# Performance work log

Hardware: AMD Instinct MI355X
Metric: run time of the kernel (lower is better)

## Reference

```python
import jax, jax.numpy as jnp
import numpy as np

B, N, CZ, CH, CA, H, TN = 1, 256, 128, 128, 32, 4, 4


def setup_inputs() -> dict:
    key = jax.random.key(0)
    ks = iter(jax.random.split(key, 64))

    def rn(shape, s=0.02):
        return jax.random.normal(next(ks), shape, dtype=jnp.float32) * s

    d = {"z": jax.random.normal(next(ks), (B, N, N, CZ), dtype=jnp.float32)}
    # Triangle multiplication params, stacked [2, ...]: idx 0 = outgoing, 1 = incoming
    d["tm_ln_in_w"] = jnp.ones((2, CZ)); d["tm_ln_in_b"] = jnp.zeros((2, CZ))
    for nm, shp in [("ap", (2, CZ, CH)), ("ag", (2, CZ, CH)), ("bp", (2, CZ, CH)),
                    ("bg", (2, CZ, CH)), ("g", (2, CZ, CZ)), ("zo", (2, CH, CZ))]:
        d[f"tm_{nm}_w"] = rn(shp)
        d[f"tm_{nm}_b"] = jnp.zeros((2, shp[-1]))
    d["tm_lnout_w"] = jnp.ones((2, CH)); d["tm_lnout_b"] = jnp.zeros((2, CH))
    # Triangle attention params, stacked [2, ...]: idx 0 = start, 1 = end
    d["ta_ln_w"] = jnp.ones((2, CZ)); d["ta_ln_b"] = jnp.zeros((2, CZ))
    d["ta_q_w"] = rn((2, CZ, H * CA)); d["ta_k_w"] = rn((2, CZ, H * CA)); d["ta_v_w"] = rn((2, CZ, H * CA))
    d["ta_b_w"] = rn((2, CZ, H))
    d["ta_g_w"] = rn((2, CZ, H * CA)); d["ta_g_b"] = jnp.zeros((2, H * CA))
    d["ta_o_w"] = rn((2, H * CA, CZ)); d["ta_o_b"] = jnp.zeros((2, CZ))
    # Pair transition
    d["pt_ln_w"] = jnp.ones((CZ,)); d["pt_ln_b"] = jnp.zeros((CZ,))
    d["pt_1_w"] = rn((CZ, TN * CZ)); d["pt_1_b"] = jnp.zeros((TN * CZ,))
    d["pt_2_w"] = rn((TN * CZ, CZ)); d["pt_2_b"] = jnp.zeros((CZ,))
    return d


def _ln(x, w, b, eps=1e-5):
    m = jnp.mean(x, axis=-1, keepdims=True)
    v = jnp.mean(jnp.square(x - m), axis=-1, keepdims=True)
    return (x - m) * jax.lax.rsqrt(v + eps) * w + b


def _tri_mul(z, lnw, lnb, apw, apb, agw, agb, bpw, bpb, bgw, bgb, gw, gb,
             lnow, lnob, zw, zb, outgoing):
    x = _ln(z, lnw, lnb)
    a = jax.nn.sigmoid(x @ agw + agb) * (x @ apw + apb)  # [B,I,J,CH]
    b = jax.nn.sigmoid(x @ bgw + bgb) * (x @ bpw + bpb)
    eq = 'bikc,bjkc->bijc' if outgoing else 'bkic,bkjc->bijc'
    t = jnp.einsum(eq, a, b)  # O(N^3 * CH)
    t = _ln(t, lnow, lnob) @ zw + zb
    return t * jax.nn.sigmoid(x @ gw + gb)


def _tri_att(z, lnw, lnb, qw, kw, vw, bw, gw, gb, ow, ob):
    Bz, I, J, _ = z.shape
    x = _ln(z, lnw, lnb)
    # triangle bias [B,1,H,I,J] (broadcast over query row)
    bias = jnp.einsum('bijc,ch->bhij', x, bw)[:, None]
    q = (x @ qw).reshape(Bz, I, J, H, CA).transpose(0, 1, 3, 2, 4) / np.float32(np.sqrt(CA))
    k = (x @ kw).reshape(Bz, I, J, H, CA).transpose(0, 1, 3, 2, 4)
    v = (x @ vw).reshape(Bz, I, J, H, CA).transpose(0, 1, 3, 2, 4)
    a = jnp.einsum('bihqc,bihkc->bihqk', q, k) + bias  # [B,I,H,J,J]
    p = jax.nn.softmax(a, axis=-1)
    o = jnp.einsum('bihqk,bihkc->bihqc', p, v).transpose(0, 1, 3, 2, 4).reshape(Bz, I, J, H * CA)
    o = o * jax.nn.sigmoid(x @ gw + gb)
    return o @ ow + ob


def reference(z, tm_ln_in_w, tm_ln_in_b, tm_ap_w, tm_ap_b, tm_ag_w, tm_ag_b,
              tm_bp_w, tm_bp_b, tm_bg_w, tm_bg_b, tm_g_w, tm_g_b,
              tm_lnout_w, tm_lnout_b, tm_zo_w, tm_zo_b,
              ta_ln_w, ta_ln_b, ta_q_w, ta_k_w, ta_v_w, ta_b_w,
              ta_g_w, ta_g_b, ta_o_w, ta_o_b,
              pt_ln_w, pt_ln_b, pt_1_w, pt_1_b, pt_2_w, pt_2_b):
    def tm(zz, i, outgoing):
        return _tri_mul(zz, tm_ln_in_w[i], tm_ln_in_b[i], tm_ap_w[i], tm_ap_b[i],
                        tm_ag_w[i], tm_ag_b[i], tm_bp_w[i], tm_bp_b[i],
                        tm_bg_w[i], tm_bg_b[i], tm_g_w[i], tm_g_b[i],
                        tm_lnout_w[i], tm_lnout_b[i], tm_zo_w[i], tm_zo_b[i], outgoing)

    def ta(zz, i):
        return _tri_att(zz, ta_ln_w[i], ta_ln_b[i], ta_q_w[i], ta_k_w[i], ta_v_w[i],
                        ta_b_w[i], ta_g_w[i], ta_g_b[i], ta_o_w[i], ta_o_b[i])

    z = z + tm(z, 0, True)          # triangle mult outgoing + residual (dropout = eval identity)
    z = z + tm(z, 1, False)         # triangle mult incoming + residual
    z = z + ta(z, 0)                # triangle attention (starting node)
    zt = jnp.swapaxes(z, 1, 2)      # transpose for ending-node attention
    zt = zt + ta(zt, 1)
    z = jnp.swapaxes(zt, 1, 2)
    x = _ln(z, pt_ln_w, pt_ln_b)    # pair transition
    z = z + (jax.nn.relu(x @ pt_1_w + pt_1_b) @ pt_2_w + pt_2_b)
    return z
```

## Files before the change

kernel.cpp:

```cpp
#include <hip/hip_runtime.h>
#include <math.h>

#define N_  256
#define NN  65536
#define CZ  128
#define CH  128
#define H_  4
#define CA  32

typedef __attribute__((ext_vector_type(8))) short bf16x8;
typedef __attribute__((ext_vector_type(4))) float f32x4;

__device__ __forceinline__ float sigmoidf_(float x){ return 1.f/(1.f+__expf(-x)); }

__device__ __forceinline__ short f2b(float f){
  unsigned u = __float_as_uint(f);
  unsigned r = (u + 0x7fffu + ((u>>16)&1u)) >> 16;
  return (short)r;
}
__device__ __forceinline__ float b2f(short s){
  unsigned u = ((unsigned)(unsigned short)s) << 16;
  return __uint_as_float(u);
}
__device__ __forceinline__ unsigned pk_bf16(float lo, float hi){
  unsigned r;
  asm volatile("v_cvt_pk_bf16_f32 %0, %1, %2" : "=v"(r) : "v"(lo), "v"(hi));
  return r;
}

__device__ __forceinline__ void glds16(const void* g, const void* l){
  __builtin_amdgcn_global_load_lds((const __attribute__((address_space(1))) void*)g,
                                   (__attribute__((address_space(3))) void*)l, 16, 0, 0);
}

__device__ __forceinline__ float wave_red_sum(float v){
  #pragma unroll
  for(int o=32;o>0;o>>=1) v += __shfl_xor(v,o,64);
  return v;
}

__device__ __forceinline__ int Gperm(int t, int m){
  return ((t>>1)<<5) + ((m>>2)<<3) + ((t&1)<<2) + (m&3);
}

__global__ void __launch_bounds__(256) prep_weights(
    const float* tm_ag, const float* tm_ap, const float* tm_bg, const float* tm_bp,
    const float* tm_g, const float* tm_zo,
    const float* ta_q, const float* ta_k, const float* ta_v, const float* ta_g, const float* ta_o,
    const float* pt1, const float* pt2, short* Wf){
  int tid = threadIdx.x;
  int g = blockIdx.x*4 + (tid>>6);
  int l = tid & 63;
  int s = blockIdx.y;
  const float* src; int ldn = 128, koff = 0, noff = 0;
  if (s < 12){
    int i = s/6, w = s - i*6;
    switch(w){ case 0: src=tm_ag; break; case 1: src=tm_ap; break; case 2: src=tm_bg; break;
               case 3: src=tm_bp; break; case 4: src=tm_g;  break; default: src=tm_zo; }
    src += i*16384;
  } else if (s < 22){
    int t2 = s-12; int i = t2/5, w = t2 - i*5;
    switch(w){ case 0: src=ta_q; break; case 1: src=ta_k; break; case 2: src=ta_v; break;
               case 3: src=ta_g; break; default: src=ta_o; }
    src += i*16384;
  } else if (s < 26){
    src = pt1; ldn = 512; noff = (s-22)*128;
  } else {
    src = pt2; koff = (s-26)*128;
  }
  int nt = g>>2, ks = g&3;
  int n = noff + nt*16 + (l&15);
  int kb = koff + ks*32 + (l>>4)*8;
  short tmp[8];
  #pragma unroll
  for (int e=0;e<8;e++) tmp[e] = f2b(src[(size_t)(kb+e)*ldn + n]);
  short* dst = Wf + s*16384 + ((nt*4+ks)*64 + l)*8;
  *(short4*)dst     = *(short4*)&tmp[0];
  *(short4*)(dst+4) = *(short4*)&tmp[4];
}

template<bool TRANS>
__global__ void __launch_bounds__(256) ln_x(const float* __restrict__ in,
                                            const float* __restrict__ w,
                                            const float* __restrict__ b,
                                            short* __restrict__ out){
  int wid  = threadIdx.x >> 6;
  int lane = threadIdx.x & 63;
  int row  = blockIdx.x*4 + wid;
  int irow;
  if (TRANS){ int i = row >> 8, j = row & 255; irow = (j<<8) | i; } else irow = row;
  float v0 = in[(size_t)irow*CZ + lane];
  float v1 = in[(size_t)irow*CZ + lane + 64];
  float m  = wave_red_sum(v0+v1) * (1.f/128.f);
  float d0 = v0-m, d1 = v1-m;
  float var = wave_red_sum(d0*d0 + d1*d1) * (1.f/128.f);
  float r = rsqrtf(var + 1e-5f);
  out[(size_t)row*CZ + lane]      = f2b(d0*r*w[lane]    + b[lane]);
  out[(size_t)row*CZ + lane + 64] = f2b(d1*r*w[lane+64] + b[lane+64]);
}

__device__ __forceinline__ void stage128_8(const short* __restrict__ g, short* xs, int r0, int tid){
  #pragma unroll
  for (int m=0;m<4;++m){
    int d = m*512 + tid;
    int row = d>>4, cw = d&15;
    glds16(&g[(size_t)(r0+row)*128 + ((cw ^ (row&15))<<3)], xs + (size_t)(d & ~63)*8);
  }
}

__device__ __forceinline__ bf16x8 ldsA(const short* xs, int row, int ch){
  return *(const bf16x8*)&xs[row*128 + ((ch ^ (row&15))<<3)];
}

__device__ __forceinline__ void gemm_coreP(const short* xs, const short* __restrict__ wf,
                                           int wm, int wn, int l, f32x4 (&acc)[2][4]){
  #pragma unroll
  for (int kh=0; kh<2; ++kh){
    bf16x8 b[2][4];
    #pragma unroll
    for (int ks2=0; ks2<2; ++ks2)
      #pragma unroll
      for (int nt=0; nt<4; ++nt)
        b[ks2][nt] = *(const bf16x8*)&wf[(((wn*4+nt)*4 + kh*2+ks2)*64 + l)*8];
    #pragma unroll
    for (int ks2=0; ks2<2; ++ks2){
      bf16x8 a[2];
      #pragma unroll
      for (int mt=0; mt<2; ++mt)
        a[mt] = ldsA(xs, wm*32 + mt*16 + (l&15), (kh*2+ks2)*4 + (l>>4));
      #pragma unroll
      for (int mt=0; mt<2; ++mt)
        #pragma unroll
        for (int nt=0; nt<4; ++nt)
          acc[mt][nt] = __builtin_amdgcn_mfma_f32_16x16x32_bf16(a[mt], b[ks2][nt], acc[mt][nt], 0,0,0);
    }
  }
}

#define ZERO_ACC(A) { _Pragma("unroll") for(int _a=0;_a<2;_a++) _Pragma("unroll") for(int _b=0;_b<4;_b++) A[_a][_b]=(f32x4){0,0,0,0}; }

#define GEMM_PROLOG8 \
  int tid = threadIdx.x; int r0 = blockIdx.x*128; \
  int wid = tid>>6, l = tid&63; int wm = wid>>1, wn = wid&1; (void)r0;

#define EPI8 \
  int row = wm*32 + mt*16 + ((l>>4)<<2) + reg; \
  int col = wn*64 + nt*16 + (l&15);

#define FOR_EPI for (int mt=0;mt<2;++mt) for (int nt=0;nt<4;++nt) for (int reg=0;reg<4;++reg)

__global__ void __launch_bounds__(512,4) k_quad_gate(const short* __restrict__ X,
                                                     const short* __restrict__ Wagf, const float* __restrict__ bag,
                                                     const short* __restrict__ Wapf, const float* __restrict__ bap,
                                                     const short* __restrict__ Wbgf, const float* __restrict__ bbg,
                                                     const short* __restrict__ Wbpf, const float* __restrict__ bbp,
                                                     short* __restrict__ out1, short* __restrict__ out2){
  __shared__ short xs[128*128];
  GEMM_PROLOG8
  stage128_8(X, xs, r0, tid);
  __syncthreads();
  {
    f32x4 ag[2][4], ap[2][4];
    ZERO_ACC(ag) ZERO_ACC(ap)
    gemm_coreP(xs, Wagf, wm, wn, l, ag);
    gemm_coreP(xs, Wapf, wm, wn, l, ap);
    FOR_EPI{
      EPI8
      float v = (ap[mt][nt][reg] + bap[col]) * sigmoidf_(ag[mt][nt][reg] + bag[col]);
      out1[(size_t)(r0+row)*128 + col] = f2b(v);
    }
  }
  {
    f32x4 bg2[2][4], bp2[2][4];
    ZERO_ACC(bg2) ZERO_ACC(bp2)
    gemm_coreP(xs, Wbgf, wm, wn, l, bg2);
    gemm_coreP(xs, Wbpf, wm, wn, l, bp2);
    FOR_EPI{
      EPI8
      float v = (bp2[mt][nt][reg] + bbp[col]) * sigmoidf_(bg2[mt][nt][reg] + bbg[col]);
      out2[(size_t)(r0+row)*128 + col] = f2b(v);
    }
  }
}

__global__ void __launch_bounds__(512,4) k_qkv(const short* __restrict__ X,
                                               const short* __restrict__ Wqf, float sq,
                                               const short* __restrict__ Wkf,
                                               const short* __restrict__ Wvf,
                                               const float* __restrict__ bw,
                                               short* __restrict__ out_q, short* __restrict__ out_k,
                                               short* __restrict__ Vt, float* __restrict__ BSF){
  __shared__ short xs[128*128];
  GEMM_PROLOG8
  stage128_8(X, xs, r0, tid);
  __syncthreads();
  {
    f32x4 aq[2][4], ak[2][4];
    ZERO_ACC(aq) ZERO_ACC(ak)
    gemm_coreP(xs, Wqf, wm, wn, l, aq);
    gemm_coreP(xs, Wkf, wm, wn, l, ak);
    FOR_EPI{
      EPI8
      out_q[(size_t)(r0+row)*128 + col] = f2b(aq[mt][nt][reg]*sq);
      out_k[(size_t)(r0+row)*128 + col] = f2b(ak[mt][nt][reg]);
    }
  }
  f32x4 av[2][4];
  ZERO_ACC(av)
  gemm_coreP(xs, Wvf, wm, wn, l, av);
  {
    int rl = tid & 127, hh = tid >> 7;
    float bacc = 0.f;
    #pragma unroll
    for (int ch=0; ch<16; ++ch){
      bf16x8 v = ldsA(xs, rl, ch);
      #pragma unroll
      for (int e=0;e<8;++e) bacc += b2f(v[e]) * bw[(ch*8+e)*H_ + hh];
    }
    int r = r0 + rl;
    int qq = r >> 8, j = r & 255;
    int t = ((j>>5)<<1) + ((j>>2)&1);
    int mm = (((j>>3)&3)<<2) + (j&3);
    int idx = (((hh*16 + (qq>>4))*16 + t) << 8) + (((mm>>2)*16 + (qq&15)) << 2) + (mm&3);
    BSF[idx] = bacc;
  }
  __syncthreads();
  #pragma unroll
  for (int mt=0;mt<2;++mt)
    #pragma unroll
    for (int nt=0;nt<4;++nt){
      int rb  = wm*32 + mt*16 + ((l>>4)<<2);
      int col = wn*64 + nt*16 + (l&15);
      short4 s4 = { f2b(av[mt][nt][0]), f2b(av[mt][nt][1]), f2b(av[mt][nt][2]), f2b(av[mt][nt][3]) };
      *(short4*)&xs[col*128 + (((rb>>3) ^ (col&15))<<3) + (rb&7)] = s4;
    }
  __syncthreads();
  int i = r0>>8, j0 = r0&255;
  #pragma unroll
  for (int m=0;m<4;++m){
    int d = m*512 + tid;
    int c = d>>4, ch = d&15;
    int4 val = *(const int4*)&xs[c*128 + ((ch ^ (c&15))<<3)];
    *(int4*)&Vt[(size_t)((i*4 + (c>>5))*32 + (c&31))*256 + j0 + ch*8] = val;
  }
}

__global__ void __launch_bounds__(512,4) k_tri_finish(const short* __restrict__ Tb,
                                                      const short* __restrict__ X,
                                                      const short* __restrict__ Wzf, const float* __restrict__ bz,
                                                      const short* __restrict__ Wgf, const float* __restrict__ bg,
                                                      const float* __restrict__ lnw, const float* __restrict__ lnb,
                                                      const float* __restrict__ zin, float* __restrict__ zout){
  __shared__ short tt[128*128];
  __shared__ short xs[128*128];
  __shared__ float ps[512], pq[512];
  __shared__ float mu[128], iv[128];
  GEMM_PROLOG8
  stage128_8(X, xs, r0, tid);
  #pragma unroll
  for (int m=0;m<4;++m){
    int d = m*512 + tid;
    int c = d>>4, ch = d&15;
    glds16(&Tb[(size_t)c*65536 + r0 + ch*8], tt + (size_t)(d & ~63)*8);
  }
  __syncthreads();
  int rl = tid & 127, cq = tid >> 7;
  float vals[32]; float s = 0.f, q = 0.f;
  #pragma unroll
  for (int cc=0; cc<32; ++cc){
    float v = b2f(tt[(cq*32+cc)*128 + rl]);
    vals[cc] = v; s += v; q += v*v;
  }
  ps[cq*128 + rl] = s; pq[cq*128 + rl] = q;
  __syncthreads();
  if (tid < 128){
    float ss = ps[tid]+ps[128+tid]+ps[256+tid]+ps[384+tid];
    float qq = pq[tid]+pq[128+tid]+pq[256+tid]+pq[384+tid];
    float m = ss * (1.f/128.f);
    float var = qq * (1.f/128.f) - m*m;
    mu[tid] = m; iv[tid] = rsqrtf(var + 1e-5f);
  }
  __syncthreads();
  {
    float m = mu[rl], r = iv[rl];
    #pragma unroll
    for (int chq=0; chq<4; ++chq){
      short tmp[8];
      #pragma unroll
      for (int e=0;e<8;++e){
        int cc = chq*8 + e;
        int c = cq*32 + cc;
        tmp[e] = f2b((vals[cc]-m)*r*lnw[c] + lnb[c]);
      }
      int ch = cq*4 + chq;
      *(int4*)&tt[rl*128 + ((ch ^ (rl&15))<<3)] = *(int4*)tmp;
    }
  }
  __syncthreads();
  f32x4 az[2][4], ag[2][4];
  ZERO_ACC(az) ZERO_ACC(ag)
  gemm_coreP(tt, Wzf, wm, wn, l, az);
  gemm_coreP(xs, Wgf, wm, wn, l, ag);
  FOR_EPI{
    EPI8
    size_t idx = (size_t)(r0+row)*128 + col;
    float v = (az[mt][nt][reg] + bz[col]) * sigmoidf_(ag[mt][nt][reg] + bg[col]);
    zout[idx] = zin[idx] + v;
  }
}

template<bool TRANS>
__global__ void __launch_bounds__(512,4) k_attn_out(const short* __restrict__ O,
                                                    const short* __restrict__ X,
                                                    const short* __restrict__ Wgf, const float* __restrict__ bg,
                                                    const short* __restrict__ Wof, const float* __restrict__ bo,
                                                    float* __restrict__ z){
  __shared__ short xs[128*128];
  __shared__ short os[128*128];
  GEMM_PROLOG8
  stage128_8(X, xs, r0, tid);
  #pragma unroll
  for (int m=0;m<4;++m){
    int d = m*512 + tid;
    int row = d>>4, ch = d&15;
    glds16(&O[(size_t)(r0+row)*128 + ch*8], os + (size_t)(d & ~63)*8);
  }
  __syncthreads();
  f32x4 ag[2][4];
  ZERO_ACC(ag)
  gemm_coreP(xs, Wgf, wm, wn, l, ag);
  __syncthreads();
  FOR_EPI{
    EPI8
    float ov = b2f(os[row*128 + col]);
    float v = ov * sigmoidf_(ag[mt][nt][reg] + bg[col]);
    xs[row*128 + (((col>>3) ^ (row&15))<<3) + (col&7)] = f2b(v);
  }
  __syncthreads();
  f32x4 a2[2][4];
  ZERO_ACC(a2)
  gemm_coreP(xs, Wof, wm, wn, l, a2);
  FOR_EPI{
    EPI8
    int orow = r0+row;
    int zrow = TRANS ? (((orow&255)<<8) | (orow>>8)) : orow;
    z[(size_t)zrow*128 + col] += a2[mt][nt][reg] + bo[col];
  }
}

__global__ void __launch_bounds__(512,4) k_pt(const float* __restrict__ lnw, const float* __restrict__ lnb,
                                              const short* __restrict__ W1f, const float* __restrict__ b1,
                                              const short* __restrict__ W2f, const float* __restrict__ b2,
                                              float* __restrict__ z){
  __shared__ short xs[128*128];
  __shared__ short hs[128*128];
  __shared__ float ps[512], pq[512];
  __shared__ float mu[128], iv[128];
  GEMM_PROLOG8
  int rl = tid & 127, cq = tid >> 7;
  float vals[32]; float s = 0.f, q = 0.f;
  {
    const float* zr = &z[(size_t)(r0+rl)*128 + cq*32];
    #pragma unroll
    for (int cc=0; cc<32; cc+=4){
      float4 v4 = *(const float4*)&zr[cc];
      vals[cc]=v4.x; vals[cc+1]=v4.y; vals[cc+2]=v4.z; vals[cc+3]=v4.w;
      s += v4.x+v4.y+v4.z+v4.w;
      q += v4.x*v4.x + v4.y*v4.y + v4.z*v4.z + v4.w*v4.w;
    }
  }
  ps[cq*128 + rl] = s; pq[cq*128 + rl] = q;
  __syncthreads();
  if (tid < 128){
    float ss = ps[tid]+ps[128+tid]+ps[256+tid]+ps[384+tid];
    float qq = pq[tid]+pq[128+tid]+pq[256+tid]+pq[384+tid];
    float m = ss * (1.f/128.f);
    float var = qq * (1.f/128.f) - m*m;
    mu[tid] = m; iv[tid] = rsqrtf(var + 1e-5f);
  }
  __syncthreads();
  {
    float m = mu[rl], r = iv[rl];
    #pragma unroll
    for (int chq=0; chq<4; ++chq){
      short tmp[8];
      #pragma unroll
      for (int e=0;e<8;++e){
        int cc = chq*8 + e;
        int c = cq*32 + cc;
        tmp[e] = f2b((vals[cc]-m)*r*lnw[c] + lnb[c]);
      }
      int ch = cq*4 + chq;
      *(int4*)&xs[rl*128 + ((ch ^ (rl&15))<<3)] = *(int4*)tmp;
    }
  }
  __syncthreads();
  f32x4 a2[2][4];
  ZERO_ACC(a2)
  for (int m=0;m<4;++m){
    f32x4 a1[2][4];
    ZERO_ACC(a1)
    gemm_coreP(xs, W1f + m*16384, wm, wn, l, a1);
    FOR_EPI{
      EPI8
      float v = fmaxf(a1[mt][nt][reg] + b1[m*128 + col], 0.f);
      hs[row*128 + (((col>>3) ^ (row&15))<<3) + (col&7)] = f2b(v);
    }
    __syncthreads();
    gemm_coreP(hs, W2f + m*16384, wm, wn, l, a2);
    __syncthreads();
  }
  FOR_EPI{
    EPI8
    z[(size_t)(r0+row)*128 + col] += a2[mt][nt][reg] + b2[col];
  }
}

template<bool TR>
__global__ void __launch_bounds__(256) pack_cxy(const short* __restrict__ inA, const short* __restrict__ inB,
                                                short* __restrict__ outA, short* __restrict__ outB){
  __shared__ short tile[256*144];
  const short* in = blockIdx.y ? inB : inA;
  short* out      = blockIdx.y ? outB : outA;
  int x = blockIdx.x, tid = threadIdx.x;
  #pragma unroll
  for (int m=0;m<16;++m){
    int idx = m*256 + tid;
    int y = idx>>4, c0 = (idx&15)*8;
    int r = TR ? (y*256 + x) : (x*256 + y);
    *(int4*)&tile[y*144 + c0] = *(const int4*)&in[(size_t)r*128 + c0];
  }
  __syncthreads();
  int c = tid & 127, yh = tid >> 7;
  short* ob = out + (size_t)c*65536 + x*256 + yh*128;
  #pragma unroll
  for (int yc=0; yc<16; ++yc){
    short tmp[8];
    #pragma unroll
    for (int e=0;e<8;e++) tmp[e] = tile[(yh*128 + yc*8 + e)*144 + c];
    *(int4*)&ob[yc*8] = *(int4*)tmp;
  }
}

__global__ void __launch_bounds__(512,4) k_einsum(const short* __restrict__ Ab,
                                                  const short* __restrict__ Bb,
                                                  short* __restrict__ Tb){
  __shared__ short as[2][128*64];
  __shared__ short bs[2][128*64];
  int c = blockIdx.z;
  int i0 = blockIdx.x*128, j0 = blockIdx.y*128;
  const short* A = Ab + (size_t)c*65536;
  const short* B = Bb + (size_t)c*65536;
  int tid = threadIdx.x;
  int wid = tid>>6, l = tid&63; int wm = wid>>1, wn = wid&1;
  f32x4 acc[2][4];
  ZERO_ACC(acc)

  #define ESTAGE(buf, kt) { \
    _Pragma("unroll") \
    for (int m_=0;m_<2;++m_){ \
      int d_ = m_*512 + tid; \
      int row_ = d_>>3, cw_ = d_&7; \
      glds16(&A[(size_t)(i0+row_)*256 + (kt)*64 + ((cw_ ^ (row_&7))<<3)], &as[buf][(d_ & ~63)*8]); \
      glds16(&B[(size_t)(j0+row_)*256 + (kt)*64 + ((cw_ ^ (row_&7))<<3)], &bs[buf][(d_ & ~63)*8]); \
    } }

  ESTAGE(0, 0)
  __syncthreads();
  for (int kt=0; kt<4; ++kt){
    int cur = kt & 1;
    if (kt < 3) ESTAGE(cur^1, kt+1)
    #pragma unroll
    for (int ks=0; ks<2; ++ks){
      bf16x8 a[2], b[4];
      #pragma unroll
      for (int mt=0; mt<2; ++mt){
        int row = wm*32 + mt*16 + (l&15);
        int ch  = (ks*4 + (l>>4)) ^ (row&7);
        a[mt] = *(const bf16x8*)&as[cur][row*64 + ch*8];
      }
      #pragma unroll
      for (int nt=0; nt<4; ++nt){
        int row = wn*64 + nt*16 + (l&15);
        int ch  = (ks*4 + (l>>4)) ^ (row&7);
        b[nt] = *(const bf16x8*)&bs[cur][row*64 + ch*8];
      }
      #pragma unroll
      for (int mt=0; mt<2; ++mt)
        #pragma unroll
        for (int nt=0; nt<4; ++nt)
          acc[mt][nt] = __builtin_amdgcn_mfma_f32_16x16x32_bf16(a[mt], b[nt], acc[mt][nt], 0,0,0);
    }
    __syncthreads();
  }
  short* To = Tb + (size_t)c*65536;
  FOR_EPI{
    int row = wm*32 + mt*16 + ((l>>4)<<2) + reg;
    int col = wn*64 + nt*16 + (l&15);
    To[(size_t)(i0+row)*256 + j0+col] = f2b(acc[mt][nt][reg]);
  }
}

__global__ void __launch_bounds__(256, 3) attn_mfma(const short* __restrict__ Qg,
                                                    const short* __restrict__ Kg,
                                                    const short* __restrict__ Vt,
                                                    const float* __restrict__ BSF,
                                                    short* __restrict__ O){
  __shared__ short Kf[8192];
  __shared__ short Vf[8192];
  int i = blockIdx.x, h = blockIdx.y;
  int tid = threadIdx.x;
  #pragma unroll
  for (int m=0;m<4;++m){
    int d = m*256 + tid;
    int t = d>>6, ll = d&63;
    glds16(&Kg[(size_t)(i*N_ + Gperm(t, ll&15))*CH + h*CA + ((ll>>4)<<3)],
           Kf + (size_t)(d & ~63)*8);
    glds16(&Vt[(size_t)(((i*H_ + h)*CA) + ((t>>3)<<4) + (ll&15))*N_ + ((t&7)<<5) + ((ll>>4)<<3)],
           Vf + (size_t)(d & ~63)*8);
  }
  __syncthreads();

  int wid = tid >> 6, l = tid & 63;
  int lg = l >> 4, ln = l & 15;

  for (int ss=0; ss<4; ++ss){
    int sub = wid*4 + ss;
    bf16x8 qfrag = *(const bf16x8*)&Qg[(size_t)(i*N_ + sub*16 + ln)*CH + h*CA + (lg<<3)];
    const float* bb = BSF + (size_t)(h*16 + sub)*4096 + (l<<2);
    f32x4 acc[16];
    #pragma unroll
    for (int t=0;t<16;t++) acc[t] = *(const f32x4*)&bb[t<<8];
    #pragma unroll
    for (int t=0;t<16;t++){
      bf16x8 kf = *(const bf16x8*)&Kf[t*512 + l*8];
      acc[t] = __builtin_amdgcn_mfma_f32_16x16x32_bf16(kf, qfrag, acc[t], 0,0,0);
    }
    float mx = -1e30f;
    #pragma unroll
    for (int t=0;t<16;t++)
      mx = fmaxf(mx, fmaxf(fmaxf(acc[t][0],acc[t][1]), fmaxf(acc[t][2],acc[t][3])));
    mx = fmaxf(mx, __shfl_xor(mx,16,64));
    mx = fmaxf(mx, __shfl_xor(mx,32,64));
    float sum = 0.f;
    #pragma unroll
    for (int t=0;t<16;t++){
      #pragma unroll
      for (int r=0;r<4;r++){ float p = __expf(acc[t][r]-mx); acc[t][r]=p; sum += p; }
    }
    sum += __shfl_xor(sum,16,64);
    sum += __shfl_xor(sum,32,64);
    float iv = 1.0f / sum;
    bf16x8 pf[8];
    #pragma unroll
    for (int jt=0;jt<8;jt++){
      int4 w4;
      w4.x = pk_bf16(acc[2*jt  ][0], acc[2*jt  ][1]);
      w4.y = pk_bf16(acc[2*jt  ][2], acc[2*jt  ][3]);
      w4.z = pk_bf16(acc[2*jt+1][0], acc[2*jt+1][1]);
      w4.w = pk_bf16(acc[2*jt+1][2], acc[2*jt+1][3]);
      pf[jt] = *(bf16x8*)&w4;
    }
    #pragma unroll
    for (int ct=0; ct<2; ++ct){
      f32x4 oe = {0.f,0.f,0.f,0.f}, oo = {0.f,0.f,0.f,0.f};
      #pragma unroll
      for (int jt=0;jt<8;jt+=2){
        bf16x8 ve = *(const bf16x8*)&Vf[((ct*8 + jt  )*64 + l)*8];
        bf16x8 vo = *(const bf16x8*)&Vf[((ct*8 + jt+1)*64 + l)*8];
        oe = __builtin_amdgcn_mfma_f32_16x16x32_bf16(ve, pf[jt  ], oe, 0,0,0);
        oo = __builtin_amdgcn_mfma_f32_16x16x32_bf16(vo, pf[jt+1], oo, 0,0,0);
      }
      int q = sub*16 + ln;
      int c = ct*16 + lg*4;
      short4 ov = { f2b((oe[0]+oo[0])*iv), f2b((oe[1]+oo[1])*iv),
                    f2b((oe[2]+oo[2])*iv), f2b((oe[3]+oo[3])*iv) };
      *(short4*)&O[(size_t)(i*N_ + q)*CH + h*CA + c] = ov;
    }
  }
}

extern "C" void kernel_launch(void* const* d_in, const int* in_sizes, int n_in,
                              void* d_out, int out_size, void* d_ws, size_t ws_size,
                              hipStream_t stream) {
  const float* z_in      = (const float*)d_in[0];
  const float* tm_lnin_w = (const float*)d_in[1];
  const float* tm_lnin_b = (const float*)d_in[2];
  const float* tm_ap_w   = (const float*)d_in[3];
  const float* tm_ap_b   = (const float*)d_in[4];
  const float* tm_ag_w   = (const float*)d_in[5];
  const float* tm_ag_b   = (const float*)d_in[6];
  const float* tm_bp_w   = (const float*)d_in[7];
  const float* tm_bp_b   = (const float*)d_in[8];
  const float* tm_bg_w   = (const float*)d_in[9];
  const float* tm_bg_b   = (const float*)d_in[10];
  const float* tm_g_w    = (const float*)d_in[11];
  const float* tm_g_b    = (const float*)d_in[12];
  const float* tm_zo_w   = (const float*)d_in[13];
  const float* tm_zo_b   = (const float*)d_in[14];
  const float* tm_lno_w  = (const float*)d_in[15];
  const float* tm_lno_b  = (const float*)d_in[16];
  const float* ta_ln_w   = (const float*)d_in[17];
  const float* ta_ln_b   = (const float*)d_in[18];
  const float* ta_q_w    = (const float*)d_in[19];
  const float* ta_k_w    = (const float*)d_in[20];
  const float* ta_v_w    = (const float*)d_in[21];
  const float* ta_b_w    = (const float*)d_in[22];
  const float* ta_g_w    = (const float*)d_in[23];
  const float* ta_g_b    = (const float*)d_in[24];
  const float* ta_o_w    = (const float*)d_in[25];
  const float* ta_o_b    = (const float*)d_in[26];
  const float* pt_ln_w   = (const float*)d_in[27];
  const float* pt_ln_b   = (const float*)d_in[28];
  const float* pt_1_w    = (const float*)d_in[29];
  const float* pt_1_b    = (const float*)d_in[30];
  const float* pt_2_w    = (const float*)d_in[31];
  const float* pt_2_b    = (const float*)d_in[32];

  float* z  = (float*)d_out;
  char* base = (char*)d_ws;
  const size_t MB = 1u<<20;
  short* wf  = (short*)base;
  short* Xb  = (short*)(base + 1*MB);
  short* R1  = (short*)(base + 17*MB);
  short* R2  = (short*)(base + 33*MB);
  short* R3  = (short*)(base + 49*MB);
  short* R4  = (short*)(base + 65*MB);
  short* Tb  = (short*)(base + 81*MB);
  float* BSF = (float*)(base + 113*MB);

  #define SL(s) (wf + (size_t)(s)*16384)

  prep_weights<<<dim3(8,30), 256, 0, stream>>>(tm_ag_w, tm_ap_w, tm_bg_w, tm_bp_w,
                                               tm_g_w, tm_zo_w,
                                               ta_q_w, ta_k_w, ta_v_w, ta_g_w, ta_o_w,
                                               pt_1_w, pt_2_w, wf);

  for (int i=0;i<2;i++){
    const float* zsrc = (i==0) ? z_in : z;
    ln_x<false><<<NN/4, 256, 0, stream>>>(zsrc, tm_lnin_w+i*CZ, tm_lnin_b+i*CZ, Xb);
    k_quad_gate<<<NN/128, 512, 0, stream>>>(Xb, SL(i*6+0), tm_ag_b+i*CH, SL(i*6+1), tm_ap_b+i*CH,
                                            SL(i*6+2), tm_bg_b+i*CH, SL(i*6+3), tm_bp_b+i*CH,
                                            R1, R2);
    if (i==0) pack_cxy<false><<<dim3(256,2), 256, 0, stream>>>(R1, R2, R3, R4);
    else      pack_cxy<true ><<<dim3(256,2), 256, 0, stream>>>(R1, R2, R3, R4);
    k_einsum<<<dim3(2,2,128), 512, 0, stream>>>(R3, R4, Tb);
    k_tri_finish<<<NN/128, 512, 0, stream>>>(Tb, Xb, SL(i*6+5), tm_zo_b+i*CZ,
                                             SL(i*6+4), tm_g_b+i*CZ,
                                             tm_lno_w+i*CH, tm_lno_b+i*CH, zsrc, z);
  }

  for (int i=0;i<2;i++){
    if (i==0) ln_x<false><<<NN/4, 256, 0, stream>>>(z, ta_ln_w, ta_ln_b, Xb);
    else      ln_x<true ><<<NN/4, 256, 0, stream>>>(z, ta_ln_w+CZ, ta_ln_b+CZ, Xb);
    k_qkv<<<NN/128, 512, 0, stream>>>(Xb, SL(12+i*5+0), 0.17677669529663687f,
                                      SL(12+i*5+1), SL(12+i*5+2), ta_b_w+i*CZ*H_,
                                      R1, R2, R3, BSF);
    attn_mfma<<<dim3(N_,H_), 256, 0, stream>>>(R1, R2, R3, BSF, R4);
    if (i==0) k_attn_out<false><<<NN/128, 512, 0, stream>>>(R4, Xb, SL(12+i*5+3), ta_g_b+i*H_*CA,
                                                            SL(12+i*5+4), ta_o_b+i*CZ, z);
    else      k_attn_out<true ><<<NN/128, 512, 0, stream>>>(R4, Xb, SL(12+i*5+3), ta_g_b+i*H_*CA,
                                                            SL(12+i*5+4), ta_o_b+i*CZ, z);
  }

  k_pt<<<NN/128, 512, 0, stream>>>(pt_ln_w, pt_ln_b, SL(22), pt_1_b, SL(26), pt_2_b, z);
}
```

Measured before the change: 585.0 us.

## Stage GEMM weights through double-buffered LDS and coalesce bf16 output stores

```diff
diff --git a/kernel.cpp b/kernel.cpp
--- a/kernel.cpp
+++ b/kernel.cpp
@@ -112,28 +112,31 @@
   return *(const bf16x8*)&xs[row*128 + ((ch ^ (row&15))<<3)];
 }
 
-__device__ __forceinline__ void gemm_coreP(const short* xs, const short* __restrict__ wf,
-                                           int wm, int wn, int l, f32x4 (&acc)[2][4]){
-  #pragma unroll
-  for (int kh=0; kh<2; ++kh){
-    bf16x8 b[2][4];
-    #pragma unroll
-    for (int ks2=0; ks2<2; ++ks2)
+__device__ __forceinline__ void stageW(const short* __restrict__ wf, int h, short* wb, int tid){
+  #pragma unroll
+  for (int r=0;r<2;++r){
+    int s = r*512 + tid;
+    int ch = s>>6, ln = s&63;
+    glds16(wf + (size_t)(((ch>>1)*4 + h*2 + (ch&1))*64 + ln)*8, wb + (size_t)(s & ~63)*8);
+  }
+}
+
+__device__ __forceinline__ void core_half(const short* xs, const short* wb, int h,
+                                          int wm, int wn, int l, f32x4 (&acc)[2][4]){
+  #pragma unroll
+  for (int ks2=0; ks2<2; ++ks2){
+    bf16x8 a[2], b[4];
+    #pragma unroll
+    for (int mt=0; mt<2; ++mt)
+      a[mt] = ldsA(xs, wm*32 + mt*16 + (l&15), (h*2+ks2)*4 + (l>>4));
+    #pragma unroll
+    for (int nt=0; nt<4; ++nt)
+      b[nt] = *(const bf16x8*)&wb[(size_t)(((wn*4+nt)*2 + ks2)*64 + l)*8];
+    #pragma unroll
+    for (int mt=0; mt<2; ++mt)
       #pragma unroll
       for (int nt=0; nt<4; ++nt)
-        b[ks2][nt] = *(const bf16x8*)&wf[(((wn*4+nt)*4 + kh*2+ks2)*64 + l)*8];
-    #pragma unroll
-    for (int ks2=0; ks2<2; ++ks2){
-      bf16x8 a[2];
-      #pragma unroll
-      for (int mt=0; mt<2; ++mt)
-        a[mt] = ldsA(xs, wm*32 + mt*16 + (l&15), (kh*2+ks2)*4 + (l>>4));
-      #pragma unroll
-      for (int mt=0; mt<2; ++mt)
-        #pragma unroll
-        for (int nt=0; nt<4; ++nt)
-          acc[mt][nt] = __builtin_amdgcn_mfma_f32_16x16x32_bf16(a[mt], b[ks2][nt], acc[mt][nt], 0,0,0);
-    }
+        acc[mt][nt] = __builtin_amdgcn_mfma_f32_16x16x32_bf16(a[mt], b[nt], acc[mt][nt], 0,0,0);
   }
 }
 
@@ -148,6 +151,27 @@
   int col = wn*64 + nt*16 + (l&15);
 
 #define FOR_EPI for (int mt=0;mt<2;++mt) for (int nt=0;nt<4;++nt) for (int reg=0;reg<4;++reg)
+
+#define SCATTER_PACKED(P, LDSBUF) \
+  _Pragma("unroll") \
+  for (int mt=0;mt<2;++mt) \
+    _Pragma("unroll") \
+    for (int nt=0;nt<4;++nt){ \
+      int row0 = wm*32 + mt*16 + ((l>>4)<<2); \
+      int col  = wn*64 + nt*16 + (l&15); \
+      unsigned lo = (unsigned)P[mt][nt].x, hi = (unsigned)P[mt][nt].y; \
+      LDSBUF[(row0  )*128 + (((col>>3) ^ ((row0  )&15))<<3) + (col&7)] = (short)(lo & 0xffff); \
+      LDSBUF[(row0+1)*128 + (((col>>3) ^ ((row0+1)&15))<<3) + (col&7)] = (short)(lo >> 16); \
+      LDSBUF[(row0+2)*128 + (((col>>3) ^ ((row0+2)&15))<<3) + (col&7)] = (short)(hi & 0xffff); \
+      LDSBUF[(row0+3)*128 + (((col>>3) ^ ((row0+3)&15))<<3) + (col&7)] = (short)(hi >> 16); \
+    }
+
+#define STORE_TILE(OUT, LDSBUF) \
+  _Pragma("unroll") \
+  for (int m2=0;m2<4;++m2){ \
+    int d = m2*512 + tid; int row = d>>4, ch = d&15; \
+    *(int4*)&OUT[(size_t)(r0+row)*128 + ch*8] = *(const int4*)&LDSBUF[row*128 + ((ch ^ (row&15))<<3)]; \
+  }
 
 __global__ void __launch_bounds__(512,4) k_quad_gate(const short* __restrict__ X,
                                                      const short* __restrict__ Wagf, const float* __restrict__ bag,
@@ -155,32 +179,64 @@
                                                      const short* __restrict__ Wbgf, const float* __restrict__ bbg,
                                                      const short* __restrict__ Wbpf, const float* __restrict__ bbp,
                                                      short* __restrict__ out1, short* __restrict__ out2){
-  __shared__ short xs[128*128];
+  __shared__ short xs[16384];
+  __shared__ short wb[2][8192];
+  short* wbf = &wb[0][0];
   GEMM_PROLOG8
+  stageW(Wagf, 0, wb[0], tid);
   stage128_8(X, xs, r0, tid);
   __syncthreads();
+  int2 o1[2][4], o2[2][4];
   {
     f32x4 ag[2][4], ap[2][4];
     ZERO_ACC(ag) ZERO_ACC(ap)
-    gemm_coreP(xs, Wagf, wm, wn, l, ag);
-    gemm_coreP(xs, Wapf, wm, wn, l, ap);
-    FOR_EPI{
-      EPI8
-      float v = (ap[mt][nt][reg] + bap[col]) * sigmoidf_(ag[mt][nt][reg] + bag[col]);
-      out1[(size_t)(r0+row)*128 + col] = f2b(v);
-    }
+    stageW(Wagf, 1, wb[1], tid); core_half(xs, wb[0], 0, wm, wn, l, ag); __syncthreads();
+    stageW(Wapf, 0, wb[0], tid); core_half(xs, wb[1], 1, wm, wn, l, ag); __syncthreads();
+    stageW(Wapf, 1, wb[1], tid); core_half(xs, wb[0], 0, wm, wn, l, ap); __syncthreads();
+    stageW(Wbgf, 0, wb[0], tid); core_half(xs, wb[1], 1, wm, wn, l, ap); __syncthreads();
+    #pragma unroll
+    for (int mt=0;mt<2;++mt)
+      #pragma unroll
+      for (int nt=0;nt<4;++nt){
+        int col = wn*64 + nt*16 + (l&15);
+        float bgc = bag[col], bpc = bap[col];
+        float v0 = (ap[mt][nt][0]+bpc)*sigmoidf_(ag[mt][nt][0]+bgc);
+        float v1 = (ap[mt][nt][1]+bpc)*sigmoidf_(ag[mt][nt][1]+bgc);
+        float v2 = (ap[mt][nt][2]+bpc)*sigmoidf_(ag[mt][nt][2]+bgc);
+        float v3 = (ap[mt][nt][3]+bpc)*sigmoidf_(ag[mt][nt][3]+bgc);
+        o1[mt][nt].x = (int)pk_bf16(v0,v1);
+        o1[mt][nt].y = (int)pk_bf16(v2,v3);
+      }
   }
   {
     f32x4 bg2[2][4], bp2[2][4];
     ZERO_ACC(bg2) ZERO_ACC(bp2)
-    gemm_coreP(xs, Wbgf, wm, wn, l, bg2);
-    gemm_coreP(xs, Wbpf, wm, wn, l, bp2);
-    FOR_EPI{
-      EPI8
-      float v = (bp2[mt][nt][reg] + bbp[col]) * sigmoidf_(bg2[mt][nt][reg] + bbg[col]);
-      out2[(size_t)(r0+row)*128 + col] = f2b(v);
-    }
-  }
+    stageW(Wbgf, 1, wb[1], tid); core_half(xs, wb[0], 0, wm, wn, l, bg2); __syncthreads();
+    stageW(Wbpf, 0, wb[0], tid); core_half(xs, wb[1], 1, wm, wn, l, bg2); __syncthreads();
+    stageW(Wbpf, 1, wb[1], tid); core_half(xs, wb[0], 0, wm, wn, l, bp2); __syncthreads();
+    core_half(xs, wb[1], 1, wm, wn, l, bp2);
+    #pragma unroll
+    for (int mt=0;mt<2;++mt)
+      #pragma unroll
+      for (int nt=0;nt<4;++nt){
+        int col = wn*64 + nt*16 + (l&15);
+        float bgc = bbg[col], bpc = bbp[col];
+        float v0 = (bp2[mt][nt][0]+bpc)*sigmoidf_(bg2[mt][nt][0]+bgc);
+        float v1 = (bp2[mt][nt][1]+bpc)*sigmoidf_(bg2[mt][nt][1]+bgc);
+        float v2 = (bp2[mt][nt][2]+bpc)*sigmoidf_(bg2[mt][nt][2]+bgc);
+        float v3 = (bp2[mt][nt][3]+bpc)*sigmoidf_(bg2[mt][nt][3]+bgc);
+        o2[mt][nt].x = (int)pk_bf16(v0,v1);
+        o2[mt][nt].y = (int)pk_bf16(v2,v3);
+      }
+  }
+  __syncthreads();
+  SCATTER_PACKED(o1, wbf)
+  __syncthreads();
+  STORE_TILE(out1, wbf)
+  __syncthreads();
+  SCATTER_PACKED(o2, wbf)
+  __syncthreads();
+  STORE_TILE(out2, wbf)
 }
 
 __global__ void __launch_bounds__(512,4) k_qkv(const short* __restrict__ X,
@@ -190,24 +246,40 @@
                                                const float* __restrict__ bw,
                                                short* __restrict__ out_q, short* __restrict__ out_k,
                                                short* __restrict__ Vt, float* __restrict__ BSF){
-  __shared__ short xs[128*128];
+  __shared__ short xs[16384];
+  __shared__ short wb[2][8192];
+  short* wbf = &wb[0][0];
   GEMM_PROLOG8
+  stageW(Wqf, 0, wb[0], tid);
   stage128_8(X, xs, r0, tid);
   __syncthreads();
+  int2 oq[2][4], ok[2][4];
   {
     f32x4 aq[2][4], ak[2][4];
     ZERO_ACC(aq) ZERO_ACC(ak)
-    gemm_coreP(xs, Wqf, wm, wn, l, aq);
-    gemm_coreP(xs, Wkf, wm, wn, l, ak);
-    FOR_EPI{
-      EPI8
-      out_q[(size_t)(r0+row)*128 + col] = f2b(aq[mt][nt][reg]*sq);
-      out_k[(size_t)(r0+row)*128 + col] = f2b(ak[mt][nt][reg]);
-    }
+    stageW(Wqf, 1, wb[1], tid); core_half(xs, wb[0], 0, wm, wn, l, aq); __syncthreads();
+    stageW(Wkf, 0, wb[0], tid); core_half(xs, wb[1], 1, wm, wn, l, aq); __syncthreads();
+    #pragma unroll
+    for (int mt=0;mt<2;++mt)
+      #pragma unroll
+      for (int nt=0;nt<4;++nt){
+        oq[mt][nt].x = (int)pk_bf16(aq[mt][nt][0]*sq, aq[mt][nt][1]*sq);
+        oq[mt][nt].y = (int)pk_bf16(aq[mt][nt][2]*sq, aq[mt][nt][3]*sq);
+      }
+    stageW(Wkf, 1, wb[1], tid); core_half(xs, wb[0], 0, wm, wn, l, ak); __syncthreads();
+    stageW(Wvf, 0, wb[0], tid); core_half(xs, wb[1], 1, wm, wn, l, ak); __syncthreads();
+    #pragma unroll
+    for (int mt=0;mt<2;++mt)
+      #pragma unroll
+      for (int nt=0;nt<4;++nt){
+        ok[mt][nt].x = (int)pk_bf16(ak[mt][nt][0], ak[mt][nt][1]);
+        ok[mt][nt].y = (int)pk_bf16(ak[mt][nt][2], ak[mt][nt][3]);
+      }
   }
   f32x4 av[2][4];
   ZERO_ACC(av)
-  gemm_coreP(xs, Wvf, wm, wn, l, av);
+  stageW(Wvf, 1, wb[1], tid); core_half(xs, wb[0], 0, wm, wn, l, av); __syncthreads();
+  core_half(xs, wb[1], 1, wm, wn, l, av);
   {
     int rl = tid & 127, hh = tid >> 7;
     float bacc = 0.f;
@@ -243,19 +315,28 @@
     int4 val = *(const int4*)&xs[c*128 + ((ch ^ (c&15))<<3)];
     *(int4*)&Vt[(size_t)((i*4 + (c>>5))*32 + (c&31))*256 + j0 + ch*8] = val;
   }
-}
-
-__global__ void __launch_bounds__(512,4) k_tri_finish(const short* __restrict__ Tb,
+  SCATTER_PACKED(oq, wbf)
+  __syncthreads();
+  STORE_TILE(out_q, wbf)
+  __syncthreads();
+  SCATTER_PACKED(ok, wbf)
+  __syncthreads();
+  STORE_TILE(out_k, wbf)
+}
+
+__global__ void __launch_bounds__(512,2) k_tri_finish(const short* __restrict__ Tb,
                                                       const short* __restrict__ X,
                                                       const short* __restrict__ Wzf, const float* __restrict__ bz,
                                                       const short* __restrict__ Wgf, const float* __restrict__ bg,
                                                       const float* __restrict__ lnw, const float* __restrict__ lnb,
                                                       const float* __restrict__ zin, float* __restrict__ zout){
-  __shared__ short tt[128*128];
-  __shared__ short xs[128*128];
+  __shared__ short tt[16384];
+  __shared__ short xs[16384];
+  __shared__ short wb[2][8192];
   __shared__ float ps[512], pq[512];
   __shared__ float mu[128], iv[128];
   GEMM_PROLOG8
+  stageW(Wzf, 0, wb[0], tid);
   stage128_8(X, xs, r0, tid);
   #pragma unroll
   for (int m=0;m<4;++m){
@@ -299,8 +380,10 @@
   __syncthreads();
   f32x4 az[2][4], ag[2][4];
   ZERO_ACC(az) ZERO_ACC(ag)
-  gemm_coreP(tt, Wzf, wm, wn, l, az);
-  gemm_coreP(xs, Wgf, wm, wn, l, ag);
+  stageW(Wzf, 1, wb[1], tid); core_half(tt, wb[0], 0, wm, wn, l, az); __syncthreads();
+  stageW(Wgf, 0, wb[0], tid); core_half(tt, wb[1], 1, wm, wn, l, az); __syncthreads();
+  stageW(Wgf, 1, wb[1], tid); core_half(xs, wb[0], 0, wm, wn, l, ag); __syncthreads();
+  core_half(xs, wb[1], 1, wm, wn, l, ag);
   FOR_EPI{
     EPI8
     size_t idx = (size_t)(r0+row)*128 + col;
@@ -310,14 +393,16 @@
 }
 
 template<bool TRANS>
-__global__ void __launch_bounds__(512,4) k_attn_out(const short* __restrict__ O,
+__global__ void __launch_bounds__(512,2) k_attn_out(const short* __restrict__ O,
                                                     const short* __restrict__ X,
                                                     const short* __restrict__ Wgf, const float* __restrict__ bg,
                                                     const short* __restrict__ Wof, const float* __restrict__ bo,
                                                     float* __restrict__ z){
-  __shared__ short xs[128*128];
-  __shared__ short os[128*128];
+  __shared__ short xs[16384];
+  __shared__ short os[16384];
+  __shared__ short wb[2][8192];
   GEMM_PROLOG8
+  stageW(Wgf, 0, wb[0], tid);
   stage128_8(X, xs, r0, tid);
   #pragma unroll
   for (int m=0;m<4;++m){
@@ -328,8 +413,9 @@
   __syncthreads();
   f32x4 ag[2][4];
   ZERO_ACC(ag)
-  gemm_coreP(xs, Wgf, wm, wn, l, ag);
-  __syncthreads();
+  stageW(Wgf, 1, wb[1], tid); core_half(xs, wb[0], 0, wm, wn, l, ag); __syncthreads();
+  stageW(Wof, 0, wb[0], tid); core_half(xs, wb[1], 1, wm, wn, l, ag); __syncthreads();
+  stageW(Wof, 1, wb[1], tid);
   FOR_EPI{
     EPI8
     float ov = b2f(os[row*128 + col]);
@@ -339,7 +425,8 @@
   __syncthreads();
   f32x4 a2[2][4];
   ZERO_ACC(a2)
-  gemm_coreP(xs, Wof, wm, wn, l, a2);
+  core_half(xs, wb[0], 0, wm, wn, l, a2);
+  core_half(xs, wb[1], 1, wm, wn, l, a2);
   FOR_EPI{
     EPI8
     int orow = r0+row;
@@ -348,15 +435,17 @@
   }
 }
 
-__global__ void __launch_bounds__(512,4) k_pt(const float* __restrict__ lnw, const float* __restrict__ lnb,
+__global__ void __launch_bounds__(512,2) k_pt(const float* __restrict__ lnw, const float* __restrict__ lnb,
                                               const short* __restrict__ W1f, const float* __restrict__ b1,
                                               const short* __restrict__ W2f, const float* __restrict__ b2,
                                               float* __restrict__ z){
-  __shared__ short xs[128*128];
-  __shared__ short hs[128*128];
+  __shared__ short xs[16384];
+  __shared__ short hs[16384];
+  __shared__ short wb[2][8192];
   __shared__ float ps[512], pq[512];
   __shared__ float mu[128], iv[128];
   GEMM_PROLOG8
+  stageW(W1f, 0, wb[0], tid);
   int rl = tid & 127, cq = tid >> 7;
   float vals[32]; float s = 0.f, q = 0.f;
   {
@@ -400,14 +489,19 @@
   for (int m=0;m<4;++m){
     f32x4 a1[2][4];
     ZERO_ACC(a1)
-    gemm_coreP(xs, W1f + m*16384, wm, wn, l, a1);
+    stageW(W1f + m*16384, 1, wb[1], tid); core_half(xs, wb[0], 0, wm, wn, l, a1); __syncthreads();
+    stageW(W2f + m*16384, 0, wb[0], tid); core_half(xs, wb[1], 1, wm, wn, l, a1); __syncthreads();
+    stageW(W2f + m*16384, 1, wb[1], tid);
     FOR_EPI{
       EPI8
       float v = fmaxf(a1[mt][nt][reg] + b1[m*128 + col], 0.f);
       hs[row*128 + (((col>>3) ^ (row&15))<<3) + (col&7)] = f2b(v);
     }
     __syncthreads();
-    gemm_coreP(hs, W2f + m*16384, wm, wn, l, a2);
+    core_half(hs, wb[0], 0, wm, wn, l, a2);
+    __syncthreads();
+    if (m<3) stageW(W1f + (m+1)*16384, 0, wb[0], tid);
+    core_half(hs, wb[1], 1, wm, wn, l, a2);
     __syncthreads();
   }
   FOR_EPI{
```

Measured after the change: 534.9 us. -8.6%, faster.
